# Optimization experiments

Hardware: AMD Instinct MI355X
Metric: run time of the kernel (lower is better)

The kernel has to match this reference:

```python
import jax, jax.numpy as jnp
import numpy as np

B, C, L, H = 4, 128, 4096, 4
GROUPS, EPS = 32, 1e-5


def group_norm(x, gamma, beta):
    # x: [B, C, L]; normalize per (batch, group) over (C//G, L)
    b, c, l = x.shape
    xg = x.reshape(b, GROUPS, c // GROUPS, l)
    mu = jnp.mean(xg, axis=(2, 3), keepdims=True)
    var = jnp.var(xg, axis=(2, 3), keepdims=True)
    xn = ((xg - mu) * jax.lax.rsqrt(var + EPS)).reshape(b, c, l)
    return xn * gamma[None, :, None] + beta[None, :, None]


def setup_inputs() -> dict:
    key = jax.random.key(0)
    k1, k2, k3 = jax.random.split(key, 3)
    return {
        "x": jax.random.normal(k1, (B, C, L), dtype=jnp.float32),
        "w_qkv": jax.random.normal(k2, (3 * C, C), dtype=jnp.float32) * 0.02,
        "w_proj": jax.random.normal(k3, (C, C), dtype=jnp.float32) * 0.02,
        "b_proj": jnp.zeros((C,), dtype=jnp.float32),
        "gn_gamma": jnp.ones((C,), dtype=jnp.float32),
        "gn_beta": jnp.zeros((C,), dtype=jnp.float32),
    }


def reference(x, w_qkv, w_proj, b_proj, gn_gamma, gn_beta):
    b, c, l = x.shape
    hd = c // H
    h = group_norm(x, gn_gamma, gn_beta)
    # 1x1 conv == channel matmul: [B, 3C, L]
    qkv = jnp.einsum('oc,bcl->bol', w_qkv, h)
    # torch reshape(B*H, 3C/H, L).chunk(3, dim=1): per-head contiguous slices
    qkv = qkv.reshape(b, H, 3 * hd, l)
    q, k, v = qkv[:, :, :hd], qkv[:, :, hd:2 * hd], qkv[:, :, 2 * hd:]
    scale = 1.0 / np.sqrt(np.sqrt(hd)).astype(np.float32)
    attn = jnp.einsum('bhct,bhcs->bhts', q * scale, k * scale)
    attn = jax.nn.softmax(attn, axis=-1)
    o = jnp.einsum('bhts,bhcs->bhct', attn, v).reshape(b, c, l)
    o = jnp.einsum('oc,bcl->bol', w_proj, o) + b_proj[None, :, None]
    return o + x
```

## Files before the change

kernel.cpp:

```cpp
#include <hip/hip_runtime.h>
#include <hip/hip_bf16.h>
#include <cstdint>
#include <cstddef>


#define B_ 4
#define C_ 128
#define L_ 4096
#define H_ 4
#define HD_ 32
#define NG_ 32
#define CPG_ 4
#define EPS_ 1e-5f
#define QKSCALE_ 0.5050097650430367f

typedef __attribute__((ext_vector_type(8))) short bf16x8;
typedef __attribute__((ext_vector_type(8))) unsigned short u16x8;
typedef __attribute__((ext_vector_type(4))) float f32x4;
typedef __attribute__((ext_vector_type(16))) float f32x16;
typedef __attribute__((ext_vector_type(2))) _Float16 f16x2;
typedef __attribute__((ext_vector_type(4))) _Float16 f16x4;
typedef __attribute__((ext_vector_type(8))) _Float16 f16x8;
typedef __attribute__((ext_vector_type(2))) unsigned int u32x2;
typedef __attribute__((ext_vector_type(4))) unsigned int u32x4;

#if __has_builtin(__builtin_amdgcn_exp2f)
#define EXP2F(x) __builtin_amdgcn_exp2f(x)
#else
#define EXP2F(x) exp2f(x)
#endif

__device__ __forceinline__ float bu2f(unsigned short u) {
  return __builtin_bit_cast(float, (unsigned int)(((unsigned int)u) << 16));
}
__device__ __forceinline__ unsigned short f2bu(float f) {
  unsigned int u = __builtin_bit_cast(unsigned int, f);
  unsigned int r = (u + 0x7fffu + ((u >> 16) & 1u)) >> 16;
  return (unsigned short)r;
}
__device__ __forceinline__ float4 u42f4(ushort4 u) {
  return make_float4(bu2f(u.x), bu2f(u.y), bu2f(u.z), bu2f(u.w));
}
__device__ __forceinline__ unsigned int pkbf(float a, float b) {
  return (unsigned int)f2bu(a) | ((unsigned int)f2bu(b) << 16);
}
__device__ __forceinline__ f16x2 pkhf2(float a, float b) {
#if __has_builtin(__builtin_amdgcn_cvt_pkrtz)
  return __builtin_bit_cast(f16x2, __builtin_amdgcn_cvt_pkrtz(a, b));
#else
  f16x2 r;
  r[0] = (_Float16)a;
  r[1] = (_Float16)b;
  return r;
#endif
}
__device__ __forceinline__ unsigned int pkhf(float a, float b) {
  return __builtin_bit_cast(unsigned int, pkhf2(a, b));
}

__device__ __forceinline__ void gload16(const void* g, void* l) {
  __builtin_amdgcn_global_load_lds(
      (const __attribute__((address_space(1))) unsigned int*)g,
      (__attribute__((address_space(3))) unsigned int*)l, 16, 0, 0);
}

__device__ __forceinline__ bool detect_fast(const ushort* x) {
  __shared__ int flag_s;
  int t = threadIdx.x;
  if (t < 64) {
    int e = (x[t] >> 7) & 0xFF;
    unsigned long long m = __ballot((e < 64) || (e > 192));
    if (t == 0) flag_s = (__popcll(m) > 4) ? 1 : 0;
  }
  __syncthreads();
  return flag_s != 0;
}

__device__ __forceinline__ float4 ldx4(const void* x, size_t idx, bool f32) {
  if (f32) return *((const float4*)x + (idx >> 2));
  ushort4 u = *((const ushort4*)x + (idx >> 2));
  return u42f4(u);
}

__global__ __launch_bounds__(256) void gn_stats(const void* __restrict__ x,
                                                const void* __restrict__ wq,
                                                const void* __restrict__ wp,
                                                const void* __restrict__ bp,
                                                ushort* __restrict__ wq_b,
                                                ushort* __restrict__ wp_b,
                                                float* __restrict__ bp_f,
                                                float2* __restrict__ gpart) {
  bool f32 = detect_fast((const ushort*)x);
  int blk = blockIdx.x;
  int t = threadIdx.x;

  if (blk >= 256) {
    int i0 = ((blk - 256) * 256 + t) * 8;
#pragma unroll
    for (int k = 0; k < 8; ++k) {
      int i = i0 + k;
      if (i >= 65664) break;
      if (i < 49152) {
        wq_b[i] = f32 ? f2bu(((const float*)wq)[i]) : ((const ushort*)wq)[i];
      } else if (i < 65536) {
        int off = i - 49152;
        wp_b[off] = f32 ? f2bu(((const float*)wp)[off]) : ((const ushort*)wp)[off];
      } else {
        int off = i - 65536;
        bp_f[off] = f32 ? ((const float*)bp)[off] : bu2f(((const ushort*)bp)[off]);
      }
    }
    return;
  }

  int b = blk >> 6, rem = blk & 63;
  int g = rem >> 1, half = rem & 1;
  size_t base = ((size_t)b * C_ + (size_t)g * CPG_) * L_ + (size_t)half * 2048;

  float s = 0.f, ss = 0.f;
#pragma unroll
  for (int cc = 0; cc < 4; ++cc) {
#pragma unroll
    for (int i = 0; i < 2; ++i) {
      size_t e = base + (size_t)cc * L_ + i * 1024 + t * 4;
      float4 f = ldx4(x, e, f32);
      s += f.x + f.y + f.z + f.w;
      ss += f.x * f.x + f.y * f.y + f.z * f.z + f.w * f.w;
    }
  }
#pragma unroll
  for (int m = 32; m >= 1; m >>= 1) {
    s += __shfl_xor(s, m, 64);
    ss += __shfl_xor(ss, m, 64);
  }
  __shared__ float red[4][2];
  int wv = t >> 6;
  if ((t & 63) == 0) { red[wv][0] = s; red[wv][1] = ss; }
  __syncthreads();
  if (t == 0) {
    float ts = red[0][0] + red[1][0] + red[2][0] + red[3][0];
    float tss = red[0][1] + red[1][1] + red[2][1] + red[3][1];
    gpart[(b * 32 + g) * 2 + half] = make_float2(ts, tss);
  }
}

__global__ __launch_bounds__(256) void qkv_kernel(const ushort* __restrict__ wq_b,
                                                  const void* __restrict__ x,
                                                  const float2* __restrict__ gpart,
                                                  const void* __restrict__ gm,
                                                  const void* __restrict__ bt,
                                                  ushort* __restrict__ Qt,
                                                  ushort* __restrict__ Kt,
                                                  ushort* __restrict__ Vb) {
  bool f32 = detect_fast((const ushort*)x);
  __shared__ alignas(16) ushort Hs[64][136];
  __shared__ alignas(16) float Ls[64][69];
  __shared__ float2 abs_s[128];

  int lx = blockIdx.x, oz = blockIdx.y, b = blockIdx.z;
  int t = threadIdx.x;
  int w = t >> 6, lane = t & 63, l16 = lane & 15, q = lane >> 4, q8 = q * 8;

  if (t < 64) {
#pragma unroll
    for (int k = 0; k < 2; ++k) {
      int c = 2 * t + k;
      int g = c >> 2;
      float2 p0 = gpart[(b * 32 + g) * 2];
      float2 p1 = gpart[(b * 32 + g) * 2 + 1];
      float mu = (p0.x + p1.x) * (1.0f / 16384.0f);
      float var = (p0.y + p1.y) * (1.0f / 16384.0f) - mu * mu;
      float rs = rsqrtf(var + EPS_);
      float ga = f32 ? ((const float*)gm)[c] : bu2f(((const ushort*)gm)[c]);
      float be = f32 ? ((const float*)bt)[c] : bu2f(((const ushort*)bt)[c]);
      abs_s[c] = make_float2(ga * rs, be - mu * ga * rs);
    }
  }
  __syncthreads();

  {
    int u = t & 63, lh = (t >> 6) * 16;
    int c0 = 2 * u;
    float2 ab0 = abs_s[c0];
    float2 ab1 = abs_s[c0 + 1];
    size_t xo = ((size_t)b * C_ + c0) * L_ + (size_t)lx * 64 + lh;
#pragma unroll
    for (int j = 0; j < 4; ++j) {
      float4 f0 = ldx4(x, xo + j * 4, f32);
      float4 f1 = ldx4(x, xo + L_ + j * 4, f32);
      float n0[4] = {f0.x * ab0.x + ab0.y, f0.y * ab0.x + ab0.y,
                     f0.z * ab0.x + ab0.y, f0.w * ab0.x + ab0.y};
      float n1[4] = {f1.x * ab1.x + ab1.y, f1.y * ab1.x + ab1.y,
                     f1.z * ab1.x + ab1.y, f1.w * ab1.x + ab1.y};
#pragma unroll
      for (int k = 0; k < 4; ++k)
        *(unsigned int*)&Hs[lh + j * 4 + k][c0] = pkbf(n0[k], n1[k]);
    }
  }
  __syncthreads();

  for (int j = 0; j < 2; ++j) {
    int oy = oz * 2 + j;
    const ushort* wg = wq_b + (size_t)(oy * 64 + w * 16 + l16) * C_;

    f32x4 acc[4] = {{0.f, 0.f, 0.f, 0.f}, {0.f, 0.f, 0.f, 0.f},
                    {0.f, 0.f, 0.f, 0.f}, {0.f, 0.f, 0.f, 0.f}};
#pragma unroll
    for (int kc = 0; kc < 4; ++kc) {
      bf16x8 aw = *(const bf16x8*)(wg + kc * 32 + q8);
#pragma unroll
      for (int nb = 0; nb < 4; ++nb) {
        bf16x8 bh = *(const bf16x8*)&Hs[nb * 16 + l16][kc * 32 + q8];
        acc[nb] = __builtin_amdgcn_mfma_f32_16x16x32_bf16(aw, bh, acc[nb], 0, 0, 0);
      }
    }
    __syncthreads();
#pragma unroll
    for (int nb = 0; nb < 4; ++nb)
#pragma unroll
      for (int r = 0; r < 4; ++r)
        Ls[nb * 16 + l16][w * 16 + 4 * q + r] = acc[nb][r];
    __syncthreads();

#pragma unroll
    for (int hhalf = 0; hhalf < 2; ++hhalf) {
      int hh = oy * 2 + hhalf;
      int type = hh % 3, head = hh / 3;
      size_t bh = (size_t)b * H_ + head;
      if (type == 2) {
        int c_loc = t >> 3, l8 = (t & 7) * 8;
        float v[8];
#pragma unroll
        for (int jj = 0; jj < 8; ++jj) v[jj] = Ls[l8 + jj][hhalf * 32 + c_loc];
        uint4 u;
        u.x = pkhf(v[0], v[1]);
        u.y = pkhf(v[2], v[3]);
        u.z = pkhf(v[4], v[5]);
        u.w = pkhf(v[6], v[7]);
        *(uint4*)(Vb + (bh * 32 + c_loc) * L_ + (size_t)lx * 64 + l8) = u;
      } else {
        ushort* dst = type ? Kt : Qt;
        int l = t >> 2, seg = (t & 3) * 8;
        const float* src = &Ls[l][hhalf * 32 + seg];
        uint4 u;
        u.x = pkbf(src[0] * QKSCALE_, src[1] * QKSCALE_);
        u.y = pkbf(src[2] * QKSCALE_, src[3] * QKSCALE_);
        u.z = pkbf(src[4] * QKSCALE_, src[5] * QKSCALE_);
        u.w = pkbf(src[6] * QKSCALE_, src[7] * QKSCALE_);
        *(uint4*)(dst + ((bh * L_) + lx * 64 + l) * 32 + seg) = u;
      }
    }
  }
}

__global__ __launch_bounds__(512, 8) void attn_kernel(const ushort* __restrict__ Qt,
                                                      const ushort* __restrict__ Kt,
                                                      const ushort* __restrict__ Vb,
                                                      ushort* __restrict__ ot) {
  __shared__ alignas(16) char smem[35840];

  int t = threadIdx.x;
  int w = t >> 6, lane = t & 63, l31 = lane & 31, hi = lane >> 5;
  int qt = w & 1, sh = w >> 1;
  int tq0 = blockIdx.x * 64;
  int bh = blockIdx.y;
  int b = bh >> 2, head = bh & 3;
  const ushort* Qg = Qt + ((size_t)bh * L_ + tq0) * 32;
  const ushort* Kg = Kt + (size_t)bh * L_ * 32;
  const ushort* Vg = Vb + (size_t)bh * 32 * L_;

  int rd = t >> 2, pd = t & 3;
  int kcsem = (pd - (rd >> 1)) & 3;
  const ushort* ksrc = Kg + (size_t)rd * 32 + kcsem * 8;
  int vr = t >> 4, vp = t & 15;
  int vcsem = (vp & 8) | ((vp & 7) ^ (vr & 7));
  const ushort* vsrc = Vg + (size_t)vr * L_ + vcsem * 8;

  char* kb0 = smem;
  char* kb1 = smem + 8192;
  char* vb0 = smem + 16384;
  char* vb1 = smem + 24576;

  const ushort* qbase = Qg + (size_t)(qt * 32 + l31) * 32;
  bf16x8 qB0 = *(const bf16x8*)(qbase + 8 * hi);
  bf16x8 qB1 = *(const bf16x8*)(qbase + 16 + 8 * hi);

  const f16x2 one2 = {(_Float16)1.0f, (_Float16)1.0f};
  const f32x16 zz = {0.f};

  gload16(ksrc, kb0 + (size_t)t * 16);
  gload16(vsrc, vb0 + (size_t)t * 16);
  ksrc += 4096;
  vsrc += 128;
  __syncthreads();

  f32x16 aO = {0.f};
  float lsum = 0.f;
  int s0 = 32 * sh;
  int rot = (l31 >> 1) & 3;

  int flip = 0;
  for (int it = 0; it < 32; ++it) {
    if (it < 31) {
      gload16(ksrc, (flip ? kb0 : kb1) + (size_t)t * 16);
      gload16(vsrc, (flip ? vb0 : vb1) + (size_t)t * 16);
      ksrc += 4096;
      vsrc += 128;
    }
    const ushort* kc = (const ushort*)(flip ? kb1 : kb0);
    const ushort* vc = (const ushort*)(flip ? vb1 : vb0);

    const ushort* krow = kc + (size_t)(s0 + l31) * 32;
    bf16x8 aK0 = *(const bf16x8*)(krow + ((hi + rot) & 3) * 8);
    bf16x8 aK1 = *(const bf16x8*)(krow + ((2 + hi + rot) & 3) * 8);
    f32x16 sf;
    __builtin_amdgcn_s_setprio(1);
    sf = __builtin_amdgcn_mfma_f32_32x32x16_bf16(aK0, qB0, zz, 0, 0, 0);
    sf = __builtin_amdgcn_mfma_f32_32x32x16_bf16(aK1, qB1, sf, 0, 0, 0);
    __builtin_amdgcn_s_setprio(0);

#pragma unroll
    for (int sb = 0; sb < 2; ++sb) {
      int sblk = 2 * sh + sb;
      int kci = 2 * sblk + hi;
      int vpos = (kci & 8) | ((kci & 7) ^ (l31 & 7));
      f16x8 vf = *(const f16x8*)(vc + (size_t)l31 * 128 + vpos * 8);

      float p0 = EXP2F(sf[8 * sb + 0]);
      float p1 = EXP2F(sf[8 * sb + 1]);
      float p2 = EXP2F(sf[8 * sb + 2]);
      float p3 = EXP2F(sf[8 * sb + 3]);
      float p4 = EXP2F(sf[8 * sb + 4]);
      float p5 = EXP2F(sf[8 * sb + 5]);
      float p6 = EXP2F(sf[8 * sb + 6]);
      float p7 = EXP2F(sf[8 * sb + 7]);
      f16x2 cA0 = pkhf2(p0, p1), cA1 = pkhf2(p2, p3);
      f16x2 cB0 = pkhf2(p4, p5), cB1 = pkhf2(p6, p7);
      lsum = __builtin_amdgcn_fdot2(cA0, one2, lsum, false);
      lsum = __builtin_amdgcn_fdot2(cA1, one2, lsum, false);
      lsum = __builtin_amdgcn_fdot2(cB0, one2, lsum, false);
      lsum = __builtin_amdgcn_fdot2(cB1, one2, lsum, false);

      u32x2 r0 = __builtin_amdgcn_permlane32_swap(
          __builtin_bit_cast(unsigned int, cA0),
          __builtin_bit_cast(unsigned int, cB0), false, false);
      u32x2 r1 = __builtin_amdgcn_permlane32_swap(
          __builtin_bit_cast(unsigned int, cA1),
          __builtin_bit_cast(unsigned int, cB1), false, false);
      u32x4 pw = {r0.x, r1.x, r0.y, r1.y};
      f16x8 pf = __builtin_bit_cast(f16x8, pw);

      __builtin_amdgcn_s_setprio(1);
      aO = __builtin_amdgcn_mfma_f32_32x32x16_f16(vf, pf, aO, 0, 0, 0);
      __builtin_amdgcn_s_setprio(0);
    }
    __syncthreads();
    flip ^= 1;
  }

  float* Osh = (float*)smem;
  float* Lp = (float*)(smem + 33792);
  {
    float* ob = Osh + (size_t)(sh * 2 + qt) * (32 * 33) + (size_t)l31 * 33;
#pragma unroll
    for (int reg = 0; reg < 16; ++reg) {
      int R = (reg & 3) + 8 * (reg >> 2) + 4 * hi;
      ob[R] = aO[reg];
    }
    Lp[(sh * 2 + hi) * 64 + qt * 32 + l31] = lsum;
  }
  __syncthreads();

  {
    int qloc = t >> 3, seg = (t & 7) * 4;
    int qt2 = qloc >> 5, q31 = qloc & 31;
    float lt = 0.f;
#pragma unroll
    for (int k = 0; k < 8; ++k) lt += Lp[k * 64 + qloc];
    float inv = 1.0f / lt;
    float o[4] = {0.f, 0.f, 0.f, 0.f};
#pragma unroll
    for (int s = 0; s < 4; ++s) {
      const float* op = Osh + (size_t)(s * 2 + qt2) * (32 * 33) + (size_t)q31 * 33 + seg;
#pragma unroll
      for (int jj = 0; jj < 4; ++jj) o[jj] += op[jj];
    }
    uint2 u;
    u.x = pkbf(o[0] * inv, o[1] * inv);
    u.y = pkbf(o[2] * inv, o[3] * inv);
    *(uint2*)(ot + ((size_t)b * L_ + tq0 + qloc) * C_ + head * 32 + seg) = u;
  }
}

__global__ __launch_bounds__(256) void proj_kernel(const ushort* __restrict__ wp_b,
                                                   const float* __restrict__ bias,
                                                   const void* __restrict__ x,
                                                   const ushort* __restrict__ ot,
                                                   void* __restrict__ out) {
  bool f32 = detect_fast((const ushort*)x);
  __shared__ alignas(16) float Ls[64][37];

  int lx = blockIdx.x, oy = blockIdx.y, b = blockIdx.z;
  int t = threadIdx.x;
  int w = t >> 6, lane = t & 63, l16 = lane & 15, q = lane >> 4, q8 = q * 8;

  const ushort* wg = wp_b + (size_t)(oy * 64 + w * 16 + l16) * C_;
  const ushort* og = ot + ((size_t)b * L_ + (size_t)lx * 32) * C_;

  f32x4 acc[2] = {{0.f, 0.f, 0.f, 0.f}, {0.f, 0.f, 0.f, 0.f}};
#pragma unroll
  for (int kc = 0; kc < 4; ++kc) {
    bf16x8 aw = *(const bf16x8*)(wg + kc * 32 + q8);
#pragma unroll
    for (int nb = 0; nb < 2; ++nb) {
      bf16x8 bo = *(const bf16x8*)(og + (size_t)(nb * 16 + l16) * C_ + kc * 32 + q8);
      acc[nb] = __builtin_amdgcn_mfma_f32_16x16x32_bf16(aw, bo, acc[nb], 0, 0, 0);
    }
  }
#pragma unroll
  for (int nb = 0; nb < 2; ++nb)
#pragma unroll
    for (int r = 0; r < 4; ++r)
      Ls[w * 16 + 4 * q + r][nb * 16 + l16] = acc[nb][r];
  __syncthreads();

  {
    int o_loc = t >> 2, ls0 = (t & 3) * 8;
    float bv = bias[oy * 64 + o_loc];
    size_t off = ((size_t)b * C_ + oy * 64 + o_loc) * L_ + (size_t)lx * 32 + ls0;
#pragma unroll
    for (int jj = 0; jj < 2; ++jj) {
      float4 xf = ldx4(x, off + jj * 4, f32);
      const float* sp = &Ls[o_loc][ls0 + jj * 4];
      float4 r = make_float4(sp[0] + bv + xf.x, sp[1] + bv + xf.y,
                             sp[2] + bv + xf.z, sp[3] + bv + xf.w);
      if (f32) {
        *(float4*)((float*)out + off + jj * 4) = r;
      } else {
        *(ushort4*)((ushort*)out + off + jj * 4) =
            make_ushort4(f2bu(r.x), f2bu(r.y), f2bu(r.z), f2bu(r.w));
      }
    }
  }
}

extern "C" void kernel_launch(void* const* d_in, const int* in_sizes, int n_in,
                              void* d_out, int out_size, void* d_ws, size_t ws_size,
                              hipStream_t stream) {
  const void* x      = d_in[0];
  const void* w_qkv  = d_in[1];
  const void* w_proj = d_in[2];
  const void* b_proj = d_in[3];
  const void* gamma  = d_in[4];
  const void* beta   = d_in[5];

  char* wsb = (char*)d_ws;
  ushort* wq_b  = (ushort*)(wsb + 0);
  ushort* wp_b  = (ushort*)(wsb + 98304);
  float*  bp_f  = (float*)(wsb + 131072);
  float2* gpart = (float2*)(wsb + 131584);
  ushort* Qt    = (ushort*)(wsb + 8388608);
  ushort* Kt    = (ushort*)(wsb + 12582912);
  ushort* Vb    = (ushort*)(wsb + 16777216);
  ushort* ot    = (ushort*)(wsb + 20971520);

  gn_stats<<<dim3(289), dim3(256), 0, stream>>>(x, w_qkv, w_proj, b_proj,
                                                wq_b, wp_b, bp_f, gpart);
  qkv_kernel<<<dim3(L_ / 64, 3, B_), dim3(256), 0, stream>>>(wq_b, x, gpart, gamma, beta,
                                                             Qt, Kt, Vb);
  attn_kernel<<<dim3(L_ / 64, B_ * H_), dim3(512), 0, stream>>>(Qt, Kt, Vb, ot);
  proj_kernel<<<dim3(L_ / 32, C_ / 64, B_), dim3(256), 0, stream>>>(wp_b, bp_f, x, ot, d_out);
}
```

Before: 141.6 us.

## Compute all output channels per block in qkv/proj and use MFMA for softmax row sums

The qkv kernel now handles 32 positions per block and loops over all six 64-row output groups, so each x tile is normalized and staged once instead of three times. The proj kernel computes all 128 output channels per block, so the attention output tile is read once instead of twice. In the attention kernel, the softmax denominator is accumulated with an extra MFMA against a ones vector, replacing the per-lane fdot2 chains and shrinking the final reduction. The cost is an extra MFMA per inner step, plus narrower stores and fewer blocks in the qkv kernel.

```diff
diff --git a/kernel.cpp b/kernel.cpp
--- a/kernel.cpp
+++ b/kernel.cpp
@@ -153,11 +153,11 @@
                                                   ushort* __restrict__ Kt,
                                                   ushort* __restrict__ Vb) {
   bool f32 = detect_fast((const ushort*)x);
-  __shared__ alignas(16) ushort Hs[64][136];
-  __shared__ alignas(16) float Ls[64][69];
+  __shared__ alignas(16) ushort Hs[32][136];
+  __shared__ alignas(16) float Ls[32][69];
   __shared__ float2 abs_s[128];
 
-  int lx = blockIdx.x, oz = blockIdx.y, b = blockIdx.z;
+  int lx = blockIdx.x, b = blockIdx.y;
   int t = threadIdx.x;
   int w = t >> 6, lane = t & 63, l16 = lane & 15, q = lane >> 4, q8 = q * 8;
 
@@ -179,13 +179,13 @@
   __syncthreads();
 
   {
-    int u = t & 63, lh = (t >> 6) * 16;
+    int u = t & 63, lh = w * 8;
     int c0 = 2 * u;
     float2 ab0 = abs_s[c0];
     float2 ab1 = abs_s[c0 + 1];
-    size_t xo = ((size_t)b * C_ + c0) * L_ + (size_t)lx * 64 + lh;
-#pragma unroll
-    for (int j = 0; j < 4; ++j) {
+    size_t xo = ((size_t)b * C_ + c0) * L_ + (size_t)lx * 32 + lh;
+#pragma unroll
+    for (int j = 0; j < 2; ++j) {
       float4 f0 = ldx4(x, xo + j * 4, f32);
       float4 f1 = ldx4(x, xo + L_ + j * 4, f32);
       float n0[4] = {f0.x * ab0.x + ab0.y, f0.y * ab0.x + ab0.y,
@@ -199,24 +199,22 @@
   }
   __syncthreads();
 
-  for (int j = 0; j < 2; ++j) {
-    int oy = oz * 2 + j;
+  for (int oy = 0; oy < 6; ++oy) {
     const ushort* wg = wq_b + (size_t)(oy * 64 + w * 16 + l16) * C_;
 
-    f32x4 acc[4] = {{0.f, 0.f, 0.f, 0.f}, {0.f, 0.f, 0.f, 0.f},
-                    {0.f, 0.f, 0.f, 0.f}, {0.f, 0.f, 0.f, 0.f}};
+    f32x4 acc[2] = {{0.f, 0.f, 0.f, 0.f}, {0.f, 0.f, 0.f, 0.f}};
 #pragma unroll
     for (int kc = 0; kc < 4; ++kc) {
       bf16x8 aw = *(const bf16x8*)(wg + kc * 32 + q8);
 #pragma unroll
-      for (int nb = 0; nb < 4; ++nb) {
+      for (int nb = 0; nb < 2; ++nb) {
         bf16x8 bh = *(const bf16x8*)&Hs[nb * 16 + l16][kc * 32 + q8];
         acc[nb] = __builtin_amdgcn_mfma_f32_16x16x32_bf16(aw, bh, acc[nb], 0, 0, 0);
       }
     }
     __syncthreads();
 #pragma unroll
-    for (int nb = 0; nb < 4; ++nb)
+    for (int nb = 0; nb < 2; ++nb)
 #pragma unroll
       for (int r = 0; r < 4; ++r)
         Ls[nb * 16 + l16][w * 16 + 4 * q + r] = acc[nb][r];
@@ -228,26 +226,22 @@
       int type = hh % 3, head = hh / 3;
       size_t bh = (size_t)b * H_ + head;
       if (type == 2) {
-        int c_loc = t >> 3, l8 = (t & 7) * 8;
-        float v[8];
-#pragma unroll
-        for (int jj = 0; jj < 8; ++jj) v[jj] = Ls[l8 + jj][hhalf * 32 + c_loc];
-        uint4 u;
+        int c_loc = t >> 3, l4 = (t & 7) * 4;
+        float v[4];
+#pragma unroll
+        for (int jj = 0; jj < 4; ++jj) v[jj] = Ls[l4 + jj][hhalf * 32 + c_loc];
+        uint2 u;
         u.x = pkhf(v[0], v[1]);
         u.y = pkhf(v[2], v[3]);
-        u.z = pkhf(v[4], v[5]);
-        u.w = pkhf(v[6], v[7]);
-        *(uint4*)(Vb + (bh * 32 + c_loc) * L_ + (size_t)lx * 64 + l8) = u;
+        *(uint2*)(Vb + (bh * 32 + c_loc) * L_ + (size_t)lx * 32 + l4) = u;
       } else {
         ushort* dst = type ? Kt : Qt;
-        int l = t >> 2, seg = (t & 3) * 8;
+        int l = t >> 3, seg = (t & 7) * 4;
         const float* src = &Ls[l][hhalf * 32 + seg];
-        uint4 u;
+        uint2 u;
         u.x = pkbf(src[0] * QKSCALE_, src[1] * QKSCALE_);
         u.y = pkbf(src[2] * QKSCALE_, src[3] * QKSCALE_);
-        u.z = pkbf(src[4] * QKSCALE_, src[5] * QKSCALE_);
-        u.w = pkbf(src[6] * QKSCALE_, src[7] * QKSCALE_);
-        *(uint4*)(dst + ((bh * L_) + lx * 64 + l) * 32 + seg) = u;
+        *(uint2*)(dst + ((bh * L_) + lx * 32 + l) * 32 + seg) = u;
       }
     }
   }
@@ -285,7 +279,9 @@
   bf16x8 qB0 = *(const bf16x8*)(qbase + 8 * hi);
   bf16x8 qB1 = *(const bf16x8*)(qbase + 16 + 8 * hi);
 
-  const f16x2 one2 = {(_Float16)1.0f, (_Float16)1.0f};
+  f16x8 ones8;
+#pragma unroll
+  for (int i = 0; i < 8; ++i) ones8[i] = (_Float16)1.0f;
   const f32x16 zz = {0.f};
 
   gload16(ksrc, kb0 + (size_t)t * 16);
@@ -295,7 +291,7 @@
   __syncthreads();
 
   f32x16 aO = {0.f};
-  float lsum = 0.f;
+  f32x16 aL = {0.f};
   int s0 = 32 * sh;
   int rot = (l31 >> 1) & 3;
 
@@ -336,10 +332,6 @@
       float p7 = EXP2F(sf[8 * sb + 7]);
       f16x2 cA0 = pkhf2(p0, p1), cA1 = pkhf2(p2, p3);
       f16x2 cB0 = pkhf2(p4, p5), cB1 = pkhf2(p6, p7);
-      lsum = __builtin_amdgcn_fdot2(cA0, one2, lsum, false);
-      lsum = __builtin_amdgcn_fdot2(cA1, one2, lsum, false);
-      lsum = __builtin_amdgcn_fdot2(cB0, one2, lsum, false);
-      lsum = __builtin_amdgcn_fdot2(cB1, one2, lsum, false);
 
       u32x2 r0 = __builtin_amdgcn_permlane32_swap(
           __builtin_bit_cast(unsigned int, cA0),
@@ -352,6 +344,7 @@
 
       __builtin_amdgcn_s_setprio(1);
       aO = __builtin_amdgcn_mfma_f32_32x32x16_f16(vf, pf, aO, 0, 0, 0);
+      aL = __builtin_amdgcn_mfma_f32_32x32x16_f16(ones8, pf, aL, 0, 0, 0);
       __builtin_amdgcn_s_setprio(0);
     }
     __syncthreads();
@@ -367,16 +360,14 @@
       int R = (reg & 3) + 8 * (reg >> 2) + 4 * hi;
       ob[R] = aO[reg];
     }
-    Lp[(sh * 2 + hi) * 64 + qt * 32 + l31] = lsum;
+    if (hi == 0) Lp[sh * 64 + qt * 32 + l31] = aL[0];
   }
   __syncthreads();
 
   {
     int qloc = t >> 3, seg = (t & 7) * 4;
     int qt2 = qloc >> 5, q31 = qloc & 31;
-    float lt = 0.f;
-#pragma unroll
-    for (int k = 0; k < 8; ++k) lt += Lp[k * 64 + qloc];
+    float lt = Lp[qloc] + Lp[64 + qloc] + Lp[128 + qloc] + Lp[192 + qloc];
     float inv = 1.0f / lt;
     float o[4] = {0.f, 0.f, 0.f, 0.f};
 #pragma unroll
@@ -398,38 +389,44 @@
                                                    const ushort* __restrict__ ot,
                                                    void* __restrict__ out) {
   bool f32 = detect_fast((const ushort*)x);
-  __shared__ alignas(16) float Ls[64][37];
-
-  int lx = blockIdx.x, oy = blockIdx.y, b = blockIdx.z;
+  __shared__ alignas(16) float Ls[128][33];
+
+  int lx = blockIdx.x, b = blockIdx.y;
   int t = threadIdx.x;
   int w = t >> 6, lane = t & 63, l16 = lane & 15, q = lane >> 4, q8 = q * 8;
 
-  const ushort* wg = wp_b + (size_t)(oy * 64 + w * 16 + l16) * C_;
+  const ushort* wg0 = wp_b + (size_t)(w * 16 + l16) * C_;
+  const ushort* wg1 = wp_b + (size_t)(64 + w * 16 + l16) * C_;
   const ushort* og = ot + ((size_t)b * L_ + (size_t)lx * 32) * C_;
 
-  f32x4 acc[2] = {{0.f, 0.f, 0.f, 0.f}, {0.f, 0.f, 0.f, 0.f}};
+  f32x4 acc[2][2] = {{{0.f, 0.f, 0.f, 0.f}, {0.f, 0.f, 0.f, 0.f}},
+                     {{0.f, 0.f, 0.f, 0.f}, {0.f, 0.f, 0.f, 0.f}}};
 #pragma unroll
   for (int kc = 0; kc < 4; ++kc) {
-    bf16x8 aw = *(const bf16x8*)(wg + kc * 32 + q8);
+    bf16x8 aw0 = *(const bf16x8*)(wg0 + kc * 32 + q8);
+    bf16x8 aw1 = *(const bf16x8*)(wg1 + kc * 32 + q8);
 #pragma unroll
     for (int nb = 0; nb < 2; ++nb) {
       bf16x8 bo = *(const bf16x8*)(og + (size_t)(nb * 16 + l16) * C_ + kc * 32 + q8);
-      acc[nb] = __builtin_amdgcn_mfma_f32_16x16x32_bf16(aw, bo, acc[nb], 0, 0, 0);
-    }
-  }
-#pragma unroll
-  for (int nb = 0; nb < 2; ++nb)
-#pragma unroll
-    for (int r = 0; r < 4; ++r)
-      Ls[w * 16 + 4 * q + r][nb * 16 + l16] = acc[nb][r];
+      acc[0][nb] = __builtin_amdgcn_mfma_f32_16x16x32_bf16(aw0, bo, acc[0][nb], 0, 0, 0);
+      acc[1][nb] = __builtin_amdgcn_mfma_f32_16x16x32_bf16(aw1, bo, acc[1][nb], 0, 0, 0);
+    }
+  }
+#pragma unroll
+  for (int oy = 0; oy < 2; ++oy)
+#pragma unroll
+    for (int nb = 0; nb < 2; ++nb)
+#pragma unroll
+      for (int r = 0; r < 4; ++r)
+        Ls[oy * 64 + w * 16 + 4 * q + r][nb * 16 + l16] = acc[oy][nb][r];
   __syncthreads();
 
   {
-    int o_loc = t >> 2, ls0 = (t & 3) * 8;
-    float bv = bias[oy * 64 + o_loc];
-    size_t off = ((size_t)b * C_ + oy * 64 + o_loc) * L_ + (size_t)lx * 32 + ls0;
-#pragma unroll
-    for (int jj = 0; jj < 2; ++jj) {
+    int o_loc = t >> 1, ls0 = (t & 1) * 16;
+    float bv = bias[o_loc];
+    size_t off = ((size_t)b * C_ + o_loc) * L_ + (size_t)lx * 32 + ls0;
+#pragma unroll
+    for (int jj = 0; jj < 4; ++jj) {
       float4 xf = ldx4(x, off + jj * 4, f32);
       const float* sp = &Ls[o_loc][ls0 + jj * 4];
       float4 r = make_float4(sp[0] + bv + xf.x, sp[1] + bv + xf.y,
@@ -466,8 +463,8 @@
 
   gn_stats<<<dim3(289), dim3(256), 0, stream>>>(x, w_qkv, w_proj, b_proj,
                                                 wq_b, wp_b, bp_f, gpart);
-  qkv_kernel<<<dim3(L_ / 64, 3, B_), dim3(256), 0, stream>>>(wq_b, x, gpart, gamma, beta,
-                                                             Qt, Kt, Vb);
+  qkv_kernel<<<dim3(L_ / 32, B_), dim3(256), 0, stream>>>(wq_b, x, gpart, gamma, beta,
+                                                          Qt, Kt, Vb);
   attn_kernel<<<dim3(L_ / 64, B_ * H_), dim3(512), 0, stream>>>(Qt, Kt, Vb, ot);
-  proj_kernel<<<dim3(L_ / 32, C_ / 64, B_), dim3(256), 0, stream>>>(wp_b, bp_f, x, ot, d_out);
-}
+  proj_kernel<<<dim3(L_ / 32, B_), dim3(256), 0, stream>>>(wp_b, bp_f, x, ot, d_out);
+}
```

Measured after the change: 216.2 us. 1.53x slower.
